# Kernel optimization log

Measured on AMD Instinct MI355X. Metric: run time of the kernel, lower is better.

The kernel has to match this reference:

```python
import jax, jax.numpy as jnp
import numpy as np

N = 500_000
H = 256          # hidden_channels
A = 64           # aggr_channels
K = 5            # number of aggregators: sum, min, max, mean, std
B = 8192         # num graphs (segments)


def setup_inputs() -> dict:
    key = jax.random.key(0)
    k1, k2, k3, k4 = jax.random.split(key, 4)
    x = jax.random.normal(k1, (N, H), dtype=jnp.float32)
    batch = jnp.sort(jax.random.randint(k2, (N,), 0, B)).astype(jnp.int64)
    # Linear weights (stored input-major so forward is x @ W)
    W1 = jax.random.normal(k3, (H, A * K), dtype=jnp.float32) * (1.0 / np.sqrt(H))
    W2 = jax.random.normal(k4, (A * K, H), dtype=jnp.float32) * (1.0 / np.sqrt(A * K))
    b = jnp.zeros((H,), dtype=jnp.float32)
    return {"x": x, "batch": batch, "num_graphs": B, "W1": W1, "W2": W2, "b": b}


def reference(x, batch, num_graphs, W1, W2, b):
    # lin_aggr (no bias), then chunk into 5 pieces of width A along features
    h = x @ W1                                   # [N, 5A]
    h_sum, h_min, h_max, h_mean, h_std = jnp.split(h, K, axis=1)

    seg = batch.astype(jnp.int32)
    cnt = jax.ops.segment_sum(jnp.ones((x.shape[0], 1), x.dtype), seg,
                              num_segments=num_graphs)            # [B, 1]
    cnt = jnp.maximum(cnt, 1.0)

    z_sum = jax.ops.segment_sum(h_sum, seg, num_segments=num_graphs)
    z_min = jax.ops.segment_min(h_min, seg, num_segments=num_graphs)
    z_max = jax.ops.segment_max(h_max, seg, num_segments=num_graphs)
    z_mean = jax.ops.segment_sum(h_mean, seg, num_segments=num_graphs) / cnt
    # std via E[x^2] - E[x]^2 (PyG StdAggregation), clamped for stability
    m = jax.ops.segment_sum(h_std, seg, num_segments=num_graphs) / cnt
    m2 = jax.ops.segment_sum(h_std * h_std, seg, num_segments=num_graphs) / cnt
    z_std = jnp.sqrt(jnp.maximum(m2 - m * m, 1e-5))

    z = jnp.concatenate([z_sum, z_min, z_max, z_mean, z_std], axis=1)  # [B, 5A]
    return z @ W2 + b                                                   # [B, H]
```

## Files before the change

kernel.cpp:

```cpp
#include <hip/hip_runtime.h>
#include <hip/hip_bf16.h>
#include <float.h>
#include <stdint.h>

typedef __attribute__((ext_vector_type(8))) short bf16x8;
typedef __attribute__((ext_vector_type(4))) float f32x4;

#define NCH 320
#define NCG 20
#define CHUNK 64
#define GPG 8
#define NTHR 640

static __device__ __forceinline__ unsigned short f2bf(float f) {
    union { float f; unsigned int u; } v; v.f = f;
    unsigned int u = v.u;
    u += 0x7FFFu + ((u >> 16) & 1u);
    return (unsigned short)(u >> 16);
}

__global__ void seg_start_kernel(const int* __restrict__ batch,
                                 int* __restrict__ seg, int n, int b_gr) {
    int b = blockIdx.x * blockDim.x + threadIdx.x;
    if (b > b_gr) return;
    int lo = 0, hi = n;
    while (lo < hi) {
        int mid = (lo + hi) >> 1;
        if (batch[mid] < b) lo = mid + 1; else hi = mid;
    }
    seg[b] = lo;
}

__global__ void pack_w1_kernel(const float* __restrict__ W1,
                               unsigned short* __restrict__ w1p) {
    int idx = blockIdx.x * blockDim.x + threadIdx.x;
    if (idx >= NCG * 8 * 64) return;
    int lane = idx & 63;
    int ks = (idx >> 6) & 7;
    int cg = idx >> 9;
    int col = cg * 16 + (lane & 15);
    int kbase = ks * 32 + (lane >> 4) * 8;
    unsigned short* dst = w1p + (size_t)idx * 8;
#pragma unroll
    for (int j = 0; j < 8; ++j)
        dst[j] = f2bf(W1[(size_t)(kbase + j) * NCH + col]);
}

__global__ __launch_bounds__(NTHR)
__attribute__((amdgpu_waves_per_eu(2)))
void aggr_kernel(const float* __restrict__ x, const int* __restrict__ seg,
                 const unsigned short* __restrict__ w1p, float* __restrict__ z) {
    __shared__ unsigned short xs[2][CHUNK * 256];

    const int g0 = blockIdx.x * GPG;
    const int tid = threadIdx.x;
    const int lane = tid & 63;
    const int w = tid >> 6;
    const int wtype = w >> 1;
    const int cg0 = 2 * w;
    const int rg = lane >> 4;
    const int col = lane & 15;

    const bf16x8* wp = (const bf16x8*)w1p;
    bf16x8 Bf0[8], Bf1[8];
#pragma unroll
    for (int ks = 0; ks < 8; ++ks) {
        Bf0[ks] = wp[(cg0 * 8 + ks) * 64 + lane];
        Bf1[ks] = wp[((cg0 + 1) * 8 + ks) * 64 + lane];
    }

    int addrk[8];
#pragma unroll
    for (int ks = 0; ks < 8; ++ks)
        addrk[ks] = ((col * 512) + (rg * 16) + ks * 64) ^ ((col & 7) << 4);

    const float id0 = (wtype == 1) ? FLT_MAX : (wtype == 2) ? -FLT_MAX : 0.f;
    float s0a = id0, s0b = id0, s1a = 0.f, s1b = 0.f;

    int sgi = 0, sch = 0, sS = seg[g0], sE = seg[g0 + 1];
    int snch = max(1, (sE - sS + CHUNK - 1) >> 6);
    int cgi = 0, cch = 0, cS = sS, cE = sE, cnch = snch;
    int TC = 0;
    {
        int ps = sS;
        for (int i = 0; i < GPG; ++i) {
            int pe = seg[g0 + i + 1];
            TC += max(1, (pe - ps + CHUNK - 1) >> 6);
            ps = pe;
        }
    }
    const float4* xv = (const float4*)x;

#define ADV_S { if (++sch == snch) { sgi++; sch = 0; if (sgi < GPG) { \
            sS = seg[g0 + sgi]; sE = seg[g0 + sgi + 1]; \
            snch = max(1, (sE - sS + CHUNK - 1) >> 6); } } }

#define LD1(i, dst) { int q = tid + (i) * NTHR; int row = q >> 6; \
        dst = make_float4(0.f, 0.f, 0.f, 0.f); \
        if (((i) < 6 || q < 4096) && row < rem_) \
            dst = xv[(size_t)(base_ + row) * 64 + (q & 63)]; }

#define ST1(i, src, xb) { int q = tid + (i) * NTHR; \
        if ((i) < 6 || q < 4096) { int row = q >> 6; \
            int byt = ((row * 512) + ((q & 63) * 8)) ^ ((row & 7) << 4); \
            __hip_bfloat162 lo2 = __float22bfloat162_rn(make_float2(src.x, src.y)); \
            __hip_bfloat162 hi2 = __float22bfloat162_rn(make_float2(src.z, src.w)); \
            unsigned int ulo, uhi; \
            __builtin_memcpy(&ulo, &lo2, 4); __builtin_memcpy(&uhi, &hi2, 4); \
            *(uint2*)((char*)(xb) + byt) = make_uint2(ulo, uhi); } }

    {
        const int base_ = sS;
        const int rem_ = min(sE - base_, CHUNK);
        float4 p0, p1, p2, p3, p4, p5, p6;
        LD1(0, p0) LD1(1, p1) LD1(2, p2) LD1(3, p3) LD1(4, p4) LD1(5, p5) LD1(6, p6)
        ST1(0, p0, xs[0]) ST1(1, p1, xs[0]) ST1(2, p2, xs[0]) ST1(3, p3, xs[0])
        ST1(4, p4, xs[0]) ST1(5, p5, xs[0]) ST1(6, p6, xs[0])
    }
    ADV_S
    __syncthreads();

    int cur = 0;
    for (int t = 0; t < TC; ++t) {
        const bool more = (t + 1 < TC);
        float4 p0, p1, p2, p3, p4, p5, p6;
        if (more) {
            const int base_ = sS + (sch << 6);
            const int rem_ = min(sE - base_, CHUNK);
            LD1(0, p0) LD1(1, p1) LD1(2, p2) LD1(3, p3) LD1(4, p4) LD1(5, p5) LD1(6, p6)
        }
        const int crem = min(cE - (cS + (cch << 6)), CHUNK);
        f32x4 a00 = {0,0,0,0}, a01 = {0,0,0,0}, a10 = {0,0,0,0}, a11 = {0,0,0,0};
        f32x4 a20 = {0,0,0,0}, a21 = {0,0,0,0}, a30 = {0,0,0,0}, a31 = {0,0,0,0};
        {
            const char* pb = (const char*)xs[cur];
#pragma unroll
            for (int ks = 0; ks < 8; ++ks) {
                bf16x8 x0 = *(const bf16x8*)(pb + addrk[ks]);
                bf16x8 x1 = *(const bf16x8*)(pb + addrk[ks] + 8192);
                bf16x8 x2 = *(const bf16x8*)(pb + addrk[ks] + 16384);
                bf16x8 x3 = *(const bf16x8*)(pb + addrk[ks] + 24576);
                a00 = __builtin_amdgcn_mfma_f32_16x16x32_bf16(x0, Bf0[ks], a00, 0, 0, 0);
                a01 = __builtin_amdgcn_mfma_f32_16x16x32_bf16(x0, Bf1[ks], a01, 0, 0, 0);
                a10 = __builtin_amdgcn_mfma_f32_16x16x32_bf16(x1, Bf0[ks], a10, 0, 0, 0);
                a11 = __builtin_amdgcn_mfma_f32_16x16x32_bf16(x1, Bf1[ks], a11, 0, 0, 0);
                a20 = __builtin_amdgcn_mfma_f32_16x16x32_bf16(x2, Bf0[ks], a20, 0, 0, 0);
                a21 = __builtin_amdgcn_mfma_f32_16x16x32_bf16(x2, Bf1[ks], a21, 0, 0, 0);
                a30 = __builtin_amdgcn_mfma_f32_16x16x32_bf16(x3, Bf0[ks], a30, 0, 0, 0);
                a31 = __builtin_amdgcn_mfma_f32_16x16x32_bf16(x3, Bf1[ks], a31, 0, 0, 0);
            }
        }
#define SUM4(v) ((v)[0] + (v)[1] + (v)[2] + (v)[3])
        if (wtype == 1) {
#define MFOLD(t16, A, B) { int rb = (t16) * 16 + (rg << 2); \
            if (rb + 0 < crem) { s0a = fminf(s0a, (A)[0]); s0b = fminf(s0b, (B)[0]); } \
            if (rb + 1 < crem) { s0a = fminf(s0a, (A)[1]); s0b = fminf(s0b, (B)[1]); } \
            if (rb + 2 < crem) { s0a = fminf(s0a, (A)[2]); s0b = fminf(s0b, (B)[2]); } \
            if (rb + 3 < crem) { s0a = fminf(s0a, (A)[3]); s0b = fminf(s0b, (B)[3]); } }
            MFOLD(0, a00, a01) MFOLD(1, a10, a11) MFOLD(2, a20, a21) MFOLD(3, a30, a31)
#undef MFOLD
        } else if (wtype == 2) {
#define MFOLD(t16, A, B) { int rb = (t16) * 16 + (rg << 2); \
            if (rb + 0 < crem) { s0a = fmaxf(s0a, (A)[0]); s0b = fmaxf(s0b, (B)[0]); } \
            if (rb + 1 < crem) { s0a = fmaxf(s0a, (A)[1]); s0b = fmaxf(s0b, (B)[1]); } \
            if (rb + 2 < crem) { s0a = fmaxf(s0a, (A)[2]); s0b = fmaxf(s0b, (B)[2]); } \
            if (rb + 3 < crem) { s0a = fmaxf(s0a, (A)[3]); s0b = fmaxf(s0b, (B)[3]); } }
            MFOLD(0, a00, a01) MFOLD(1, a10, a11) MFOLD(2, a20, a21) MFOLD(3, a30, a31)
#undef MFOLD
        } else if (wtype == 4) {
            s0a += SUM4(a00) + SUM4(a10) + SUM4(a20) + SUM4(a30);
            s0b += SUM4(a01) + SUM4(a11) + SUM4(a21) + SUM4(a31);
            s1a += a00[0]*a00[0] + a00[1]*a00[1] + a00[2]*a00[2] + a00[3]*a00[3]
                 + a10[0]*a10[0] + a10[1]*a10[1] + a10[2]*a10[2] + a10[3]*a10[3]
                 + a20[0]*a20[0] + a20[1]*a20[1] + a20[2]*a20[2] + a20[3]*a20[3]
                 + a30[0]*a30[0] + a30[1]*a30[1] + a30[2]*a30[2] + a30[3]*a30[3];
            s1b += a01[0]*a01[0] + a01[1]*a01[1] + a01[2]*a01[2] + a01[3]*a01[3]
                 + a11[0]*a11[0] + a11[1]*a11[1] + a11[2]*a11[2] + a11[3]*a11[3]
                 + a21[0]*a21[0] + a21[1]*a21[1] + a21[2]*a21[2] + a21[3]*a21[3]
                 + a31[0]*a31[0] + a31[1]*a31[1] + a31[2]*a31[2] + a31[3]*a31[3];
        } else {
            s0a += SUM4(a00) + SUM4(a10) + SUM4(a20) + SUM4(a30);
            s0b += SUM4(a01) + SUM4(a11) + SUM4(a21) + SUM4(a31);
        }
#undef SUM4
        if (cch == cnch - 1) {
            float v0a = s0a, v0b = s0b, v1a = s1a, v1b = s1b;
            if (wtype == 1) {
                v0a = fminf(v0a, __shfl_xor(v0a, 16)); v0a = fminf(v0a, __shfl_xor(v0a, 32));
                v0b = fminf(v0b, __shfl_xor(v0b, 16)); v0b = fminf(v0b, __shfl_xor(v0b, 32));
            } else if (wtype == 2) {
                v0a = fmaxf(v0a, __shfl_xor(v0a, 16)); v0a = fmaxf(v0a, __shfl_xor(v0a, 32));
                v0b = fmaxf(v0b, __shfl_xor(v0b, 16)); v0b = fmaxf(v0b, __shfl_xor(v0b, 32));
            } else {
                v0a += __shfl_xor(v0a, 16); v0a += __shfl_xor(v0a, 32);
                v0b += __shfl_xor(v0b, 16); v0b += __shfl_xor(v0b, 32);
                if (wtype == 4) {
                    v1a += __shfl_xor(v1a, 16); v1a += __shfl_xor(v1a, 32);
                    v1b += __shfl_xor(v1b, 16); v1b += __shfl_xor(v1b, 32);
                }
            }
            if (lane < 16) {
                float* zg = z + (size_t)(g0 + cgi) * 384;
                if (wtype < 4) {
                    zg[wtype * 64 + (cg0 & 3) * 16 + lane] = v0a;
                    zg[wtype * 64 + ((cg0 + 1) & 3) * 16 + lane] = v0b;
                } else {
                    zg[256 + (cg0 - 16) * 16 + lane] = v0a;
                    zg[256 + (cg0 - 15) * 16 + lane] = v0b;
                    zg[320 + (cg0 - 16) * 16 + lane] = v1a;
                    zg[320 + (cg0 - 15) * 16 + lane] = v1b;
                }
            }
            s0a = id0; s0b = id0; s1a = 0.f; s1b = 0.f;
        }
        if (++cch == cnch) {
            cgi++; cch = 0;
            if (cgi < GPG) {
                cS = seg[g0 + cgi]; cE = seg[g0 + cgi + 1];
                cnch = max(1, (cE - cS + CHUNK - 1) >> 6);
            }
        }
        if (more) {
            unsigned short* xb = xs[cur ^ 1];
            ST1(0, p0, xb) ST1(1, p1, xb) ST1(2, p2, xb) ST1(3, p3, xb)
            ST1(4, p4, xb) ST1(5, p5, xb) ST1(6, p6, xb)
            ADV_S
            __syncthreads();
        }
        cur ^= 1;
    }
#undef ADV_S
#undef LD1
#undef ST1
}

__global__ __launch_bounds__(256) void k2_kernel(
    const float* __restrict__ z, const int* __restrict__ seg,
    const float* __restrict__ W2, const float* __restrict__ bias,
    float* __restrict__ out) {
    __shared__ float zf[320][16];
    const int g0 = blockIdx.x * 16;
    const int tid = threadIdx.x;
    for (int idx = tid; idx < 16 * 320; idx += 256) {
        int c = idx >> 4;
        int m = idx & 15;
        int g = g0 + m;
        float cnt = (float)max(1, seg[g + 1] - seg[g]);
        const float* zg = z + (size_t)g * 384;
        int a = c >> 6, cc = c & 63;
        float val;
        if (a == 0) val = zg[cc];
        else if (a == 1) val = zg[64 + cc];
        else if (a == 2) val = zg[128 + cc];
        else if (a == 3) val = zg[192 + cc] / cnt;
        else {
            float m1 = zg[256 + cc] / cnt;
            float m2 = zg[320 + cc] / cnt;
            val = sqrtf(fmaxf(m2 - m1 * m1, 1e-5f));
        }
        zf[c][m] = val;
    }
    __syncthreads();
    float acc[16];
#pragma unroll
    for (int m = 0; m < 16; ++m) acc[m] = 0.f;
    for (int k = 0; k < 320; ++k) {
        float wv = W2[(size_t)k * 256 + tid];
#pragma unroll
        for (int m = 0; m < 16; ++m) acc[m] += zf[k][m] * wv;
    }
    float bv = bias[tid];
#pragma unroll
    for (int m = 0; m < 16; ++m)
        out[(size_t)(g0 + m) * 256 + tid] = acc[m] + bv;
}

extern "C" void kernel_launch(void* const* d_in, const int* in_sizes, int n_in,
                              void* d_out, int out_size, void* d_ws, size_t ws_size,
                              hipStream_t stream) {
    const float* x = (const float*)d_in[0];
    const int* batch = (const int*)d_in[1];
    const float* W1 = (const float*)d_in[3];
    const float* W2 = (const float*)d_in[4];
    const float* bias = (const float*)d_in[5];

    const int n = in_sizes[1];
    const int b_gr = out_size / 256;

    char* ws = (char*)d_ws;
    unsigned short* w1p = (unsigned short*)ws;
    int* seg = (int*)(ws + 163840);
    float* z = (float*)(ws + 196864);

    seg_start_kernel<<<(b_gr + 256) / 256, 256, 0, stream>>>(batch, seg, n, b_gr);
    pack_w1_kernel<<<(NCG * 8 * 64 + 255) / 256, 256, 0, stream>>>(W1, w1p);
    aggr_kernel<<<b_gr / GPG, NTHR, 0, stream>>>(x, seg, w1p, z);
    k2_kernel<<<b_gr / 16, 256, 0, stream>>>(z, seg, W2, bias, (float*)d_out);
}
```

Before: 333.0 us.

## Spread std column groups across 8 waves and triple-buffer x chunks

The block shrinks from 10 waves to 8. Each wave now also computes one std column group for half of the chunk rows, so the std work is split across all waves and combined with atomicAdd into z, which is zeroed by a new memset. Shared memory grows from two buffers to three, rotating so a buffer is not overwritten right after it is read. This aims to balance MFMA work and give each thread a full load-store pattern, at the cost of more registers per wave, atomics, and an extra memset launch.

```diff
diff --git a/kernel.cpp b/kernel.cpp
--- a/kernel.cpp
+++ b/kernel.cpp
@@ -10,7 +10,7 @@
 #define NCG 20
 #define CHUNK 64
 #define GPG 8
-#define NTHR 640
+#define NTHR 512
 
 static __device__ __forceinline__ unsigned short f2bf(float f) {
     union { float f; unsigned int u; } v; v.f = f;
@@ -50,23 +50,28 @@
 __attribute__((amdgpu_waves_per_eu(2)))
 void aggr_kernel(const float* __restrict__ x, const int* __restrict__ seg,
                  const unsigned short* __restrict__ w1p, float* __restrict__ z) {
-    __shared__ unsigned short xs[2][CHUNK * 256];
+    __shared__ unsigned short xs[3 * CHUNK * 256];
 
     const int g0 = blockIdx.x * GPG;
     const int tid = threadIdx.x;
     const int lane = tid & 63;
     const int w = tid >> 6;
+    const int cg0 = 2 * w;
     const int wtype = w >> 1;
-    const int cg0 = 2 * w;
+    const int sthalf = w >> 2;
     const int rg = lane >> 4;
     const int col = lane & 15;
 
     const bf16x8* wp = (const bf16x8*)w1p;
-    bf16x8 Bf0[8], Bf1[8];
+    bf16x8 Bm0[8], Bm1[8], Bs[8];
 #pragma unroll
     for (int ks = 0; ks < 8; ++ks) {
-        Bf0[ks] = wp[(cg0 * 8 + ks) * 64 + lane];
-        Bf1[ks] = wp[((cg0 + 1) * 8 + ks) * 64 + lane];
+        Bm0[ks] = wp[(cg0 * 8 + ks) * 64 + lane];
+        Bm1[ks] = wp[((cg0 + 1) * 8 + ks) * 64 + lane];
+        Bs[ks]  = wp[((16 + (w & 3)) * 8 + ks) * 64 + lane];
+        asm volatile("" : "+v"(Bm0[ks]));
+        asm volatile("" : "+v"(Bm1[ks]));
+        asm volatile("" : "+v"(Bs[ks]));
     }
 
     int addrk[8];
@@ -75,7 +80,8 @@
         addrk[ks] = ((col * 512) + (rg * 16) + ks * 64) ^ ((col & 7) << 4);
 
     const float id0 = (wtype == 1) ? FLT_MAX : (wtype == 2) ? -FLT_MAX : 0.f;
-    float s0a = id0, s0b = id0, s1a = 0.f, s1b = 0.f;
+    float s0a = id0, s0b = id0;
+    float ss0 = 0.f, ss1 = 0.f;
 
     int sgi = 0, sch = 0, sS = seg[g0], sE = seg[g0 + 1];
     int snch = max(1, (sE - sS + CHUNK - 1) >> 6);
@@ -97,57 +103,66 @@
 
 #define LD1(i, dst) { int q = tid + (i) * NTHR; int row = q >> 6; \
         dst = make_float4(0.f, 0.f, 0.f, 0.f); \
-        if (((i) < 6 || q < 4096) && row < rem_) \
-            dst = xv[(size_t)(base_ + row) * 64 + (q & 63)]; }
-
-#define ST1(i, src, xb) { int q = tid + (i) * NTHR; \
-        if ((i) < 6 || q < 4096) { int row = q >> 6; \
-            int byt = ((row * 512) + ((q & 63) * 8)) ^ ((row & 7) << 4); \
-            __hip_bfloat162 lo2 = __float22bfloat162_rn(make_float2(src.x, src.y)); \
-            __hip_bfloat162 hi2 = __float22bfloat162_rn(make_float2(src.z, src.w)); \
-            unsigned int ulo, uhi; \
-            __builtin_memcpy(&ulo, &lo2, 4); __builtin_memcpy(&uhi, &hi2, 4); \
-            *(uint2*)((char*)(xb) + byt) = make_uint2(ulo, uhi); } }
+        if (row < rem_) dst = xv[(size_t)(base_ + row) * 64 + (q & 63)]; }
+
+#define ST1(i, src, xb) { int q = tid + (i) * NTHR; int row = q >> 6; \
+        int byt = ((row * 512) + ((q & 63) * 8)) ^ ((row & 7) << 4); \
+        __hip_bfloat162 lo2 = __float22bfloat162_rn(make_float2(src.x, src.y)); \
+        __hip_bfloat162 hi2 = __float22bfloat162_rn(make_float2(src.z, src.w)); \
+        unsigned int ulo, uhi; \
+        __builtin_memcpy(&ulo, &lo2, 4); __builtin_memcpy(&uhi, &hi2, 4); \
+        *(uint2*)((xb) + byt) = make_uint2(ulo, uhi); }
 
     {
         const int base_ = sS;
         const int rem_ = min(sE - base_, CHUNK);
-        float4 p0, p1, p2, p3, p4, p5, p6;
-        LD1(0, p0) LD1(1, p1) LD1(2, p2) LD1(3, p3) LD1(4, p4) LD1(5, p5) LD1(6, p6)
-        ST1(0, p0, xs[0]) ST1(1, p1, xs[0]) ST1(2, p2, xs[0]) ST1(3, p3, xs[0])
-        ST1(4, p4, xs[0]) ST1(5, p5, xs[0]) ST1(6, p6, xs[0])
+        float4 p0, p1, p2, p3, p4, p5, p6, p7;
+        LD1(0, p0) LD1(1, p1) LD1(2, p2) LD1(3, p3)
+        LD1(4, p4) LD1(5, p5) LD1(6, p6) LD1(7, p7)
+        char* xb = (char*)xs;
+        ST1(0, p0, xb) ST1(1, p1, xb) ST1(2, p2, xb) ST1(3, p3, xb)
+        ST1(4, p4, xb) ST1(5, p5, xb) ST1(6, p6, xb) ST1(7, p7, xb)
     }
     ADV_S
     __syncthreads();
 
-    int cur = 0;
+    int bc = 0, bwi = 1;
     for (int t = 0; t < TC; ++t) {
         const bool more = (t + 1 < TC);
-        float4 p0, p1, p2, p3, p4, p5, p6;
+        float4 p0, p1, p2, p3, p4, p5, p6, p7;
         if (more) {
             const int base_ = sS + (sch << 6);
             const int rem_ = min(sE - base_, CHUNK);
-            LD1(0, p0) LD1(1, p1) LD1(2, p2) LD1(3, p3) LD1(4, p4) LD1(5, p5) LD1(6, p6)
+            LD1(0, p0) LD1(1, p1) LD1(2, p2) LD1(3, p3)
+            LD1(4, p4) LD1(5, p5) LD1(6, p6) LD1(7, p7)
         }
         const int crem = min(cE - (cS + (cch << 6)), CHUNK);
         f32x4 a00 = {0,0,0,0}, a01 = {0,0,0,0}, a10 = {0,0,0,0}, a11 = {0,0,0,0};
         f32x4 a20 = {0,0,0,0}, a21 = {0,0,0,0}, a30 = {0,0,0,0}, a31 = {0,0,0,0};
+        f32x4 as0 = {0,0,0,0}, as1 = {0,0,0,0};
         {
-            const char* pb = (const char*)xs[cur];
+            const char* pb = (const char*)xs + bc * 32768;
 #pragma unroll
             for (int ks = 0; ks < 8; ++ks) {
                 bf16x8 x0 = *(const bf16x8*)(pb + addrk[ks]);
                 bf16x8 x1 = *(const bf16x8*)(pb + addrk[ks] + 8192);
                 bf16x8 x2 = *(const bf16x8*)(pb + addrk[ks] + 16384);
                 bf16x8 x3 = *(const bf16x8*)(pb + addrk[ks] + 24576);
-                a00 = __builtin_amdgcn_mfma_f32_16x16x32_bf16(x0, Bf0[ks], a00, 0, 0, 0);
-                a01 = __builtin_amdgcn_mfma_f32_16x16x32_bf16(x0, Bf1[ks], a01, 0, 0, 0);
-                a10 = __builtin_amdgcn_mfma_f32_16x16x32_bf16(x1, Bf0[ks], a10, 0, 0, 0);
-                a11 = __builtin_amdgcn_mfma_f32_16x16x32_bf16(x1, Bf1[ks], a11, 0, 0, 0);
-                a20 = __builtin_amdgcn_mfma_f32_16x16x32_bf16(x2, Bf0[ks], a20, 0, 0, 0);
-                a21 = __builtin_amdgcn_mfma_f32_16x16x32_bf16(x2, Bf1[ks], a21, 0, 0, 0);
-                a30 = __builtin_amdgcn_mfma_f32_16x16x32_bf16(x3, Bf0[ks], a30, 0, 0, 0);
-                a31 = __builtin_amdgcn_mfma_f32_16x16x32_bf16(x3, Bf1[ks], a31, 0, 0, 0);
+                a00 = __builtin_amdgcn_mfma_f32_16x16x32_bf16(x0, Bm0[ks], a00, 0, 0, 0);
+                a01 = __builtin_amdgcn_mfma_f32_16x16x32_bf16(x0, Bm1[ks], a01, 0, 0, 0);
+                a10 = __builtin_amdgcn_mfma_f32_16x16x32_bf16(x1, Bm0[ks], a10, 0, 0, 0);
+                a11 = __builtin_amdgcn_mfma_f32_16x16x32_bf16(x1, Bm1[ks], a11, 0, 0, 0);
+                a20 = __builtin_amdgcn_mfma_f32_16x16x32_bf16(x2, Bm0[ks], a20, 0, 0, 0);
+                a21 = __builtin_amdgcn_mfma_f32_16x16x32_bf16(x2, Bm1[ks], a21, 0, 0, 0);
+                a30 = __builtin_amdgcn_mfma_f32_16x16x32_bf16(x3, Bm0[ks], a30, 0, 0, 0);
+                a31 = __builtin_amdgcn_mfma_f32_16x16x32_bf16(x3, Bm1[ks], a31, 0, 0, 0);
+                if (sthalf == 0) {
+                    as0 = __builtin_amdgcn_mfma_f32_16x16x32_bf16(x0, Bs[ks], as0, 0, 0, 0);
+                    as1 = __builtin_amdgcn_mfma_f32_16x16x32_bf16(x1, Bs[ks], as1, 0, 0, 0);
+                } else {
+                    as0 = __builtin_amdgcn_mfma_f32_16x16x32_bf16(x2, Bs[ks], as0, 0, 0, 0);
+                    as1 = __builtin_amdgcn_mfma_f32_16x16x32_bf16(x3, Bs[ks], as1, 0, 0, 0);
+                }
             }
         }
 #define SUM4(v) ((v)[0] + (v)[1] + (v)[2] + (v)[3])
@@ -167,24 +182,16 @@
             if (rb + 3 < crem) { s0a = fmaxf(s0a, (A)[3]); s0b = fmaxf(s0b, (B)[3]); } }
             MFOLD(0, a00, a01) MFOLD(1, a10, a11) MFOLD(2, a20, a21) MFOLD(3, a30, a31)
 #undef MFOLD
-        } else if (wtype == 4) {
-            s0a += SUM4(a00) + SUM4(a10) + SUM4(a20) + SUM4(a30);
-            s0b += SUM4(a01) + SUM4(a11) + SUM4(a21) + SUM4(a31);
-            s1a += a00[0]*a00[0] + a00[1]*a00[1] + a00[2]*a00[2] + a00[3]*a00[3]
-                 + a10[0]*a10[0] + a10[1]*a10[1] + a10[2]*a10[2] + a10[3]*a10[3]
-                 + a20[0]*a20[0] + a20[1]*a20[1] + a20[2]*a20[2] + a20[3]*a20[3]
-                 + a30[0]*a30[0] + a30[1]*a30[1] + a30[2]*a30[2] + a30[3]*a30[3];
-            s1b += a01[0]*a01[0] + a01[1]*a01[1] + a01[2]*a01[2] + a01[3]*a01[3]
-                 + a11[0]*a11[0] + a11[1]*a11[1] + a11[2]*a11[2] + a11[3]*a11[3]
-                 + a21[0]*a21[0] + a21[1]*a21[1] + a21[2]*a21[2] + a21[3]*a21[3]
-                 + a31[0]*a31[0] + a31[1]*a31[1] + a31[2]*a31[2] + a31[3]*a31[3];
         } else {
             s0a += SUM4(a00) + SUM4(a10) + SUM4(a20) + SUM4(a30);
             s0b += SUM4(a01) + SUM4(a11) + SUM4(a21) + SUM4(a31);
         }
+        ss0 += SUM4(as0) + SUM4(as1);
+        ss1 += as0[0]*as0[0] + as0[1]*as0[1] + as0[2]*as0[2] + as0[3]*as0[3]
+             + as1[0]*as1[0] + as1[1]*as1[1] + as1[2]*as1[2] + as1[3]*as1[3];
 #undef SUM4
         if (cch == cnch - 1) {
-            float v0a = s0a, v0b = s0b, v1a = s1a, v1b = s1b;
+            float v0a = s0a, v0b = s0b, w0 = ss0, w1 = ss1;
             if (wtype == 1) {
                 v0a = fminf(v0a, __shfl_xor(v0a, 16)); v0a = fminf(v0a, __shfl_xor(v0a, 32));
                 v0b = fminf(v0b, __shfl_xor(v0b, 16)); v0b = fminf(v0b, __shfl_xor(v0b, 32));
@@ -194,24 +201,17 @@
             } else {
                 v0a += __shfl_xor(v0a, 16); v0a += __shfl_xor(v0a, 32);
                 v0b += __shfl_xor(v0b, 16); v0b += __shfl_xor(v0b, 32);
-                if (wtype == 4) {
-                    v1a += __shfl_xor(v1a, 16); v1a += __shfl_xor(v1a, 32);
-                    v1b += __shfl_xor(v1b, 16); v1b += __shfl_xor(v1b, 32);
-                }
             }
+            w0 += __shfl_xor(w0, 16); w0 += __shfl_xor(w0, 32);
+            w1 += __shfl_xor(w1, 16); w1 += __shfl_xor(w1, 32);
             if (lane < 16) {
                 float* zg = z + (size_t)(g0 + cgi) * 384;
-                if (wtype < 4) {
-                    zg[wtype * 64 + (cg0 & 3) * 16 + lane] = v0a;
-                    zg[wtype * 64 + ((cg0 + 1) & 3) * 16 + lane] = v0b;
-                } else {
-                    zg[256 + (cg0 - 16) * 16 + lane] = v0a;
-                    zg[256 + (cg0 - 15) * 16 + lane] = v0b;
-                    zg[320 + (cg0 - 16) * 16 + lane] = v1a;
-                    zg[320 + (cg0 - 15) * 16 + lane] = v1b;
-                }
+                zg[wtype * 64 + (cg0 & 3) * 16 + lane] = v0a;
+                zg[wtype * 64 + ((cg0 & 3) + 1) * 16 + lane] = v0b;
+                atomicAdd(&zg[256 + (w & 3) * 16 + lane], w0);
+                atomicAdd(&zg[320 + (w & 3) * 16 + lane], w1);
             }
-            s0a = id0; s0b = id0; s1a = 0.f; s1b = 0.f;
+            s0a = id0; s0b = id0; ss0 = 0.f; ss1 = 0.f;
         }
         if (++cch == cnch) {
             cgi++; cch = 0;
@@ -221,13 +221,14 @@
             }
         }
         if (more) {
-            unsigned short* xb = xs[cur ^ 1];
+            char* xb = (char*)xs + bwi * 32768;
             ST1(0, p0, xb) ST1(1, p1, xb) ST1(2, p2, xb) ST1(3, p3, xb)
-            ST1(4, p4, xb) ST1(5, p5, xb) ST1(6, p6, xb)
+            ST1(4, p4, xb) ST1(5, p5, xb) ST1(6, p6, xb) ST1(7, p7, xb)
             ADV_S
             __syncthreads();
         }
-        cur ^= 1;
+        bc = bwi;
+        bwi = (bwi == 2) ? 0 : bwi + 1;
     }
 #undef ADV_S
 #undef LD1
@@ -294,6 +295,7 @@
 
     seg_start_kernel<<<(b_gr + 256) / 256, 256, 0, stream>>>(batch, seg, n, b_gr);
     pack_w1_kernel<<<(NCG * 8 * 64 + 255) / 256, 256, 0, stream>>>(W1, w1p);
+    hipMemsetAsync(z, 0, (size_t)b_gr * 384 * sizeof(float), stream);
     aggr_kernel<<<b_gr / GPG, NTHR, 0, stream>>>(x, seg, w1p, z);
     k2_kernel<<<b_gr / 16, 256, 0, stream>>>(z, seg, W2, bias, (float*)d_out);
 }
```

Measured after the change: 330.6 us. No clear change (-0.7%).
